# Performance work log

Measured on AMD Instinct MI355X. Metric: run time of the kernel, lower is better.

Reference implementation:

```python
import jax, jax.numpy as jnp
import numpy as np

G = 256       # number of graphs in batch
NPG = 400     # nodes per graph (hardcoded in module)
DEG = 32      # avg degree
FIN = 400     # input feature dim
H = 64        # hidden_channels
N = G * NPG
E = G * NPG * DEG


def _glorot(key, fan_in, fan_out):
    lim = float(np.sqrt(6.0 / (fan_in + fan_out)))
    return jax.random.uniform(key, (fan_in, fan_out), jnp.float32, -lim, lim)


def setup_inputs() -> dict:
    key = jax.random.key(0)
    ks = jax.random.split(key, 12)
    x = jax.random.normal(ks[0], (N, FIN), jnp.float32)
    # intra-graph random edges, then offset by graph id so edges never cross graphs
    src = jax.random.randint(ks[1], (G, NPG * DEG), 0, NPG)
    dst = jax.random.randint(ks[2], (G, NPG * DEG), 0, NPG)
    offs = (jnp.arange(G) * NPG)[:, None]
    edge_index = jnp.stack([(src + offs).reshape(-1), (dst + offs).reshape(-1)]).astype(jnp.int32)
    edge_weight = jax.random.uniform(ks[3], (E,), jnp.float32)
    return {
        "x": x,
        "edge_index": edge_index,
        "edge_weight": edge_weight,
        "W1": _glorot(ks[4], FIN, H), "b1": jnp.zeros((H,), jnp.float32),
        "W2": _glorot(ks[5], H, H),   "b2": jnp.zeros((H,), jnp.float32),
        "W3": _glorot(ks[6], H, H),   "b3": jnp.zeros((H,), jnp.float32),
        "Wc": _glorot(ks[7], NPG * H, H), "bc": jnp.zeros((H,), jnp.float32),
        "Wl": _glorot(ks[8], H, 2),   "bl": jnp.zeros((2,), jnp.float32),
    }


def _gcn_conv(x, W, b, row, col, norm, n):
    # PyG GCNConv: out[col] += norm * (x @ W)[row]; then + bias
    h = x @ W                                   # [n, out]
    msg = norm[:, None] * h[row]                # [E+n, out] gather + scale
    return jax.ops.segment_sum(msg, col, num_segments=n) + b


def reference(x, edge_index, edge_weight, W1, b1, W2, b2, W3, b3, Wc, bc, Wl, bl):
    n = x.shape[0]
    loop = jnp.arange(n, dtype=edge_index.dtype)
    row = jnp.concatenate([edge_index[0], loop])            # sources (with self-loops)
    col = jnp.concatenate([edge_index[1], loop])            # targets
    ew = jnp.concatenate([edge_weight, jnp.ones((n,), edge_weight.dtype)])
    # symmetric normalization: deg^{-1/2}[row] * w * deg^{-1/2}[col]
    deg = jax.ops.segment_sum(ew, col, num_segments=n)
    dinv = jnp.where(deg > 0, jax.lax.rsqrt(deg), 0.0)
    norm = dinv[row] * ew * dinv[col]

    h = jax.nn.relu(_gcn_conv(x, W1, b1, row, col, norm, n))
    h = jax.nn.relu(_gcn_conv(h, W2, b2, row, col, norm, n))
    h = _gcn_conv(h, W3, b3, row, col, norm, n)
    # per-graph flatten of 400 nodes -> lincomb (vectorized form of the Python loop)
    g = h.reshape(-1, NPG * H) @ Wc + bc        # [G, H]
    # dropout p=0.5 skipped (eval mode)
    return g @ Wl + bl                          # [G, 2]
```

## Files before the change

kernel.cpp:

```cpp
#include <hip/hip_runtime.h>
#include <hip/hip_bf16.h>
#include <stdint.h>

#define G 256
#define NPG 400
#define DEG 32
#define FIN 400
#define H 64
#define NN (G*NPG)
#define EE (G*NPG*DEG)
#define EPG (NPG*DEG)
#define CPG (EPG+NPG)
#define NTILE 25
#define ATS 420
#define HTS 72
#define MTF 26624

#define W1F_OFF 0
#define W1F_N   (13*4*64*8)
#define W2F_OFF (W1F_OFF + W1F_N)
#define W2F_N   (2*4*64*8)
#define W3F_OFF (W2F_OFF + W2F_N)
#define WCF_OFF (W3F_OFF + W2F_N)
#define WCF_N   (832*4*64*8)
#define WF_TOT  (WCF_OFF + WCF_N)

typedef __attribute__((ext_vector_type(8))) _Float16 h8;
typedef __attribute__((ext_vector_type(4))) float f32x4;

static __device__ __forceinline__ unsigned packh2(float a, float b) {
  unsigned short ua = __builtin_bit_cast(unsigned short, (_Float16)a);
  unsigned short ub = __builtin_bit_cast(unsigned short, (_Float16)b);
  return (unsigned)ua | ((unsigned)ub << 16);
}

static __device__ __forceinline__ h8 cvt8(float4 a, float4 b) {
  h8 r;
  r[0] = (_Float16)a.x; r[1] = (_Float16)a.y; r[2] = (_Float16)a.z; r[3] = (_Float16)a.w;
  r[4] = (_Float16)b.x; r[5] = (_Float16)b.y; r[6] = (_Float16)b.z; r[7] = (_Float16)b.w;
  return r;
}

__global__ __launch_bounds__(256) void kPack(
    const float* __restrict__ W1, const float* __restrict__ W2,
    const float* __restrict__ W3, const float* __restrict__ Wc,
    _Float16* __restrict__ wf)
{
  int idx = blockIdx.x*256 + threadIdx.x;
  if (idx >= WF_TOT) return;
  if (idx < W2F_OFF) {
    int i = idx;
    int j = i & 7, ln = (i >> 3) & 63, nt = (i >> 9) & 3, ks = i >> 11;
    int k = ks*32 + (ln >> 4)*8 + j, col = nt*16 + (ln & 15);
    wf[idx] = (k < FIN) ? (_Float16)W1[k*H + col] : (_Float16)0.f;
  } else if (idx < W3F_OFF) {
    int i = idx - W2F_OFF;
    int j = i & 7, ln = (i >> 3) & 63, nt = (i >> 9) & 3, ks = i >> 11;
    wf[idx] = (_Float16)W2[(ks*32 + (ln >> 4)*8 + j)*H + nt*16 + (ln & 15)];
  } else if (idx < WCF_OFF) {
    int i = idx - W3F_OFF;
    int j = i & 7, ln = (i >> 3) & 63, nt = (i >> 9) & 3, ks = i >> 11;
    wf[idx] = (_Float16)W3[(ks*32 + (ln >> 4)*8 + j)*H + nt*16 + (ln & 15)];
  } else {
    int i = idx - WCF_OFF;
    int j = i & 7, ln = (i >> 3) & 63, ntc = (i >> 9) & 3, kt = i >> 11;
    int kp = kt*32 + (ln >> 4)*8 + j;
    int nt_m = kp / 6656, rem = kp % 6656;
    int ks_m = rem >> 9, rem2 = rem & 511;
    int lane_m = rem2 >> 3, j_m = rem2 & 7;
    int node = ks_m*32 + (lane_m >> 4)*8 + j_m;
    int feat = nt_m*16 + (lane_m & 15);
    int col = ntc*16 + (ln & 15);
    wf[idx] = (node < NPG) ? (_Float16)Wc[((size_t)node*64 + feat)*64 + col]
                           : (_Float16)0.f;
  }
}

__global__ __launch_bounds__(1024) void kNorm(
    const int* __restrict__ ei, const float* __restrict__ ew,
    uint2* __restrict__ ent, uint32_t* __restrict__ boff)
{
  __shared__ float deg[NPG];
  __shared__ float dv[NPG];
  __shared__ uint32_t bcnt[32], bpos[32];
  const int g = blockIdx.x, tid = threadIdx.x;
  const int ebase = g*EPG, nbase = g*NPG;
  const int* rowp = ei;
  const int* colp = ei + EE;
  if (tid < NTILE) bcnt[tid] = 0u;
  for (int v = tid; v < NPG; v += 1024) deg[v] = 1.0f;
  __syncthreads();
  for (int e = tid; e < EPG; e += 1024) {
    int c = colp[ebase+e] - nbase;
    atomicAdd(&deg[c], ew[ebase+e]);
    atomicAdd(&bcnt[c >> 4], 1u);
  }
  __syncthreads();
  for (int v = tid; v < NPG; v += 1024) dv[v] = rsqrtf(deg[v]);
  if (tid == 0) {
    uint32_t s = 0;
    #pragma unroll
    for (int t = 0; t < NTILE; ++t) {
      uint32_t c = bcnt[t] + 16u;
      bcnt[t] = s; bpos[t] = s; s += c;
    }
  }
  __syncthreads();
  if (tid < NTILE) boff[g*32 + tid] = bcnt[tid];
  if (tid == NTILE) boff[g*32 + NTILE] = (uint32_t)CPG;
  uint2* eb = ent + (size_t)g*CPG;
  for (int e = tid; e < EPG; e += 1024) {
    int src = rowp[ebase+e] - nbase;
    int dst = colp[ebase+e] - nbase;
    float nm = dv[src] * ew[ebase+e] * dv[dst];
    uint32_t p = atomicAdd(&bpos[dst >> 4], 1u);
    eb[p] = make_uint2(((unsigned)dst << 16) | (unsigned)src, __float_as_uint(nm));
  }
  for (int v = tid; v < NPG; v += 1024) {
    uint32_t p = atomicAdd(&bpos[v >> 4], 1u);
    eb[p] = make_uint2(((unsigned)v << 16) | (unsigned)v, __float_as_uint(dv[v]*dv[v]));
  }
}

__global__ __launch_bounds__(256, 8) void kM1(
    const float* __restrict__ x, const _Float16* __restrict__ wf,
    _Float16* __restrict__ mt1)
{
  const int tid = threadIdx.x, lane = tid & 63, wave = tid >> 6;
  const int l15 = lane & 15, kgrp = lane >> 4;
  const int g = blockIdx.y, b = blockIdx.x;
  const int node_l = b*64 + wave*16 + l15;
  const int arow = (node_l < NPG) ? node_l : NPG-1;
  const float* xp = x + ((size_t)g*NPG + arow)*FIN;

  f32x4 acc[4] = {{0,0,0,0},{0,0,0,0},{0,0,0,0},{0,0,0,0}};
  for (int ks = 0; ks < 13; ++ks) {
    const int kb = ks*32 + kgrp*8;
    h8 af;
    if (kb + 8 <= FIN) {
      float4 a0 = *(const float4*)(xp + kb);
      float4 a1 = *(const float4*)(xp + kb + 4);
      af = cvt8(a0, a1);
    } else {
      h8 z;
      #pragma unroll
      for (int j = 0; j < 8; ++j) z[j] = (_Float16)0.f;
      af = z;
    }
    #pragma unroll
    for (int nt = 0; nt < 4; ++nt) {
      h8 bf = *(const h8*)&wf[W1F_OFF + (((size_t)ks*4 + nt)*64 + lane)*8];
      acc[nt] = __builtin_amdgcn_mfma_f32_16x16x32_f16(af, bf, acc[nt], 0, 0, 0);
    }
  }
  const int nd0 = b*64 + wave*16 + kgrp*4;
  if (nd0 < NPG) {
    const int ksw = nd0 >> 5, lh = (nd0 >> 3) & 3, jb = nd0 & 7;
    _Float16* mb = mt1 + (size_t)g*MTF;
    #pragma unroll
    for (int nt = 0; nt < 4; ++nt) {
      uint2 u;
      u.x = packh2(acc[nt][0], acc[nt][1]);
      u.y = packh2(acc[nt][2], acc[nt][3]);
      *(uint2*)&mb[(((size_t)nt*13 + ksw)*64 + lh*16 + l15)*8 + jb] = u;
    }
  }
}

template<int WMUL>
__global__ __launch_bounds__(256, 4) void kAgg(
    const _Float16* __restrict__ mtin, const _Float16* __restrict__ wfn,
    const float* __restrict__ bias,
    const uint2* __restrict__ ent, const uint32_t* __restrict__ boff,
    _Float16* __restrict__ out)
{
  extern __shared__ char smem[];
  float* sAT = (float*)smem;
  _Float16* sh = (_Float16*)(smem + 16*ATS*4);
  const int tid = threadIdx.x, lane = tid & 63;
  const int l15 = lane & 15, kgrp = lane >> 4;
  const int bid = blockIdx.x;
  const int g = bid & 255, t = bid >> 8;
  const int t0 = t*16;
  const int nt = tid >> 6;
  const uint2* eb = ent + (size_t)g*CPG;
  const uint32_t s0 = boff[g*32 + t], s1 = boff[g*32 + t + 1];

  h8 BF[13];
  const _Float16* mrow = mtin + (size_t)g*MTF + (size_t)nt*13*512 + lane*8;
  #pragma unroll
  for (int ks = 0; ks < 13; ++ks)
    BF[ks] = *(const h8*)(mrow + ks*512);
  const float bv = bias[nt*16 + l15];
  h8 WF2[2];
  if (WMUL) {
    WF2[0] = *(const h8*)&wfn[((size_t)(0*4 + nt)*64 + lane)*8];
    WF2[1] = *(const h8*)&wfn[((size_t)(1*4 + nt)*64 + lane)*8];
  }
  const uint32_t e0 = s0 + tid;
  uint2 E0 = make_uint2(0,0), E1 = make_uint2(0,0), E2 = make_uint2(0,0);
  if (e0       < s1) E0 = eb[e0];
  if (e0 + 256 < s1) E1 = eb[e0 + 256];
  if (e0 + 512 < s1) E2 = eb[e0 + 512];

  { float4* p = (float4*)sAT;
    for (int i = tid; i < 16*ATS/4; i += 256) p[i] = make_float4(0,0,0,0); }
  __syncthreads();

  if (e0       < s1) atomicAdd(&sAT[((int)(E0.x >> 16) - t0)*ATS + (int)(E0.x & 0xffffu)], __uint_as_float(E0.y));
  if (e0 + 256 < s1) atomicAdd(&sAT[((int)(E1.x >> 16) - t0)*ATS + (int)(E1.x & 0xffffu)], __uint_as_float(E1.y));
  if (e0 + 512 < s1) atomicAdd(&sAT[((int)(E2.x >> 16) - t0)*ATS + (int)(E2.x & 0xffffu)], __uint_as_float(E2.y));
  for (uint32_t e = e0 + 768; e < s1; e += 256) {
    uint2 E = eb[e];
    atomicAdd(&sAT[((int)(E.x >> 16) - t0)*ATS + (int)(E.x & 0xffffu)], __uint_as_float(E.y));
  }
  __syncthreads();

  f32x4 acc = {0,0,0,0};
  const float* ap = &sAT[l15*ATS];
  #pragma unroll
  for (int ks = 0; ks < 13; ++ks) {
    int kb = ks*32 + kgrp*8;
    float4 a0 = *(const float4*)(ap + kb);
    float4 a1 = *(const float4*)(ap + kb + 4);
    acc = __builtin_amdgcn_mfma_f32_16x16x32_f16(cvt8(a0, a1), BF[ks], acc, 0, 0, 0);
  }

  const int nd0 = t0 + kgrp*4;
  const int ksw = nd0 >> 5, lh = (nd0 >> 3) & 3, jb = nd0 & 7;
  _Float16* ob = out + (size_t)g*MTF;

  if (!WMUL) {
    uint2 u;
    u.x = packh2(acc[0] + bv, acc[1] + bv);
    u.y = packh2(acc[2] + bv, acc[3] + bv);
    *(uint2*)&ob[(((size_t)nt*13 + ksw)*64 + lh*16 + l15)*8 + jb] = u;
  } else {
    #pragma unroll
    for (int r = 0; r < 4; ++r)
      sh[(kgrp*4 + r)*HTS + nt*16 + l15] = (_Float16)fmaxf(acc[r] + bv, 0.f);
    __syncthreads();
    f32x4 acc2 = {0,0,0,0};
    const _Float16* hp = &sh[l15*HTS];
    acc2 = __builtin_amdgcn_mfma_f32_16x16x32_f16(*(const h8*)(hp + kgrp*8),      WF2[0], acc2, 0, 0, 0);
    acc2 = __builtin_amdgcn_mfma_f32_16x16x32_f16(*(const h8*)(hp + 32 + kgrp*8), WF2[1], acc2, 0, 0, 0);
    uint2 u;
    u.x = packh2(acc2[0], acc2[1]);
    u.y = packh2(acc2[2], acc2[3]);
    *(uint2*)&ob[(((size_t)nt*13 + ksw)*64 + lh*16 + l15)*8 + jb] = u;
  }
}

__global__ __launch_bounds__(256) void kRead(
    const _Float16* __restrict__ h3, const _Float16* __restrict__ wfc,
    float* __restrict__ gpart)
{
  const int tid = threadIdx.x, lane = tid & 63, nt = tid >> 6;
  const int l15 = lane & 15, kgrp = lane >> 4;
  const int rt = blockIdx.x & 15, kc = blockIdx.x >> 4;
  f32x4 acc = {0,0,0,0};
  const _Float16* hp = h3 + (size_t)(rt*16 + l15)*MTF;
  for (int ks = 0; ks < 26; ++ks) {
    int kt = kc*26 + ks;
    h8 af = *(const h8*)(hp + kt*32 + kgrp*8);
    h8 bf = *(const h8*)(wfc + (((size_t)kt*4 + nt)*64 + lane)*8);
    acc = __builtin_amdgcn_mfma_f32_16x16x32_f16(af, bf, acc, 0, 0, 0);
  }
  #pragma unroll
  for (int r = 0; r < 4; ++r)
    gpart[((size_t)(kc*16 + rt)*16 + kgrp*4 + r)*64 + nt*16 + l15] = acc[r];
}

__global__ __launch_bounds__(64) void k6_final(
    const float* __restrict__ gpart, const float* __restrict__ bc,
    const float* __restrict__ Wl, const float* __restrict__ bl,
    float* __restrict__ out)
{
  const int g = blockIdx.x, f = threadIdx.x;
  float s = bc[f];
  #pragma unroll 4
  for (int kc = 0; kc < 32; ++kc)
    s += gpart[((size_t)(kc*16 + (g >> 4))*16 + (g & 15))*64 + f];
  float p0 = s * Wl[f*2 + 0];
  float p1 = s * Wl[f*2 + 1];
  #pragma unroll
  for (int d = 1; d < 64; d <<= 1) {
    p0 += __shfl_xor(p0, d);
    p1 += __shfl_xor(p1, d);
  }
  if (f == 0) {
    out[g*2 + 0] = p0 + bl[0];
    out[g*2 + 1] = p1 + bl[1];
  }
}

extern "C" void kernel_launch(void* const* d_in, const int* in_sizes, int n_in,
                              void* d_out, int out_size, void* d_ws, size_t ws_size,
                              hipStream_t stream)
{
  const float* x  = (const float*)d_in[0];
  const int*   ei = (const int*)d_in[1];
  const float* ew = (const float*)d_in[2];
  const float* W1 = (const float*)d_in[3];
  const float* b1 = (const float*)d_in[4];
  const float* W2 = (const float*)d_in[5];
  const float* b2 = (const float*)d_in[6];
  const float* W3 = (const float*)d_in[7];
  const float* b3 = (const float*)d_in[8];
  const float* Wc = (const float*)d_in[9];
  const float* bc = (const float*)d_in[10];
  const float* Wl = (const float*)d_in[11];
  const float* bl = (const float*)d_in[12];
  float* out = (float*)d_out;
  (void)ws_size;

  char* ws = (char*)d_ws;
  size_t o = 0;
  uint2*     ent   = (uint2*)(ws + o);     o += (size_t)G*CPG*8;
  uint32_t*  boff  = (uint32_t*)(ws + o);  o += (size_t)G*32*4;
  _Float16*  mtA   = (_Float16*)(ws + o);  o += (size_t)G*MTF*2 + 256;
  _Float16*  mtB   = (_Float16*)(ws + o);  o += (size_t)G*MTF*2 + 256;
  _Float16*  wf    = (_Float16*)(ws + o);  o += (size_t)WF_TOT*2;
  float*     gpart = (float*)(ws + o);     o += (size_t)32*G*H*4;

  kPack<<<WF_TOT/256, 256, 0, stream>>>(W1, W2, W3, Wc, wf);
  kNorm<<<G, 1024, 0, stream>>>(ei, ew, ent, boff);
  kM1<<<dim3(7, G), 256, 0, stream>>>(x, wf, mtA);
  const int aggLds = 16*ATS*4 + 16*HTS*2;
  kAgg<1><<<NTILE*G, 256, aggLds, stream>>>(mtA, wf + W2F_OFF, b1, ent, boff, mtB);
  kAgg<1><<<NTILE*G, 256, aggLds, stream>>>(mtB, wf + W3F_OFF, b2, ent, boff, mtA);
  kAgg<0><<<NTILE*G, 256, aggLds, stream>>>(mtA, wf, b3, ent, boff, mtB);
  kRead<<<512, 256, 0, stream>>>(mtB, wf + WCF_OFF, gpart);
  k6_final<<<G, 64, 0, stream>>>(gpart, bc, Wl, bl, out);
}
```

Before: 265.6 us.

## Compress edge entries to 32 bits, coalesce x loads via LDS, split Wc packing

```diff
diff --git a/kernel.cpp b/kernel.cpp
--- a/kernel.cpp
+++ b/kernel.cpp
@@ -14,6 +14,7 @@
 #define NTILE 25
 #define ATS 420
 #define HTS 72
+#define XTS 36
 #define MTF 26624
 
 #define W1F_OFF 0
@@ -41,13 +42,12 @@
   return r;
 }
 
-__global__ __launch_bounds__(256) void kPack(
+__global__ __launch_bounds__(256) void kPackW(
     const float* __restrict__ W1, const float* __restrict__ W2,
-    const float* __restrict__ W3, const float* __restrict__ Wc,
-    _Float16* __restrict__ wf)
+    const float* __restrict__ W3, _Float16* __restrict__ wf)
 {
   int idx = blockIdx.x*256 + threadIdx.x;
-  if (idx >= WF_TOT) return;
+  if (idx >= WCF_OFF) return;
   if (idx < W2F_OFF) {
     int i = idx;
     int j = i & 7, ln = (i >> 3) & 63, nt = (i >> 9) & 3, ks = i >> 11;
@@ -57,28 +57,41 @@
     int i = idx - W2F_OFF;
     int j = i & 7, ln = (i >> 3) & 63, nt = (i >> 9) & 3, ks = i >> 11;
     wf[idx] = (_Float16)W2[(ks*32 + (ln >> 4)*8 + j)*H + nt*16 + (ln & 15)];
-  } else if (idx < WCF_OFF) {
+  } else {
     int i = idx - W3F_OFF;
     int j = i & 7, ln = (i >> 3) & 63, nt = (i >> 9) & 3, ks = i >> 11;
     wf[idx] = (_Float16)W3[(ks*32 + (ln >> 4)*8 + j)*H + nt*16 + (ln & 15)];
-  } else {
-    int i = idx - WCF_OFF;
-    int j = i & 7, ln = (i >> 3) & 63, ntc = (i >> 9) & 3, kt = i >> 11;
-    int kp = kt*32 + (ln >> 4)*8 + j;
-    int nt_m = kp / 6656, rem = kp % 6656;
+  }
+}
+
+__global__ __launch_bounds__(256) void kPackC(
+    const float* __restrict__ Wc, _Float16* __restrict__ wf)
+{
+  __shared__ _Float16 st[2048];
+  const int kt = blockIdx.x, tid = threadIdx.x;
+  #pragma unroll
+  for (int it = 0; it < 8; ++it) {
+    int r = it*4 + (tid >> 6);
+    int col = tid & 63;
+    int kp = kt*32 + r;
+    int nt_m = kp/6656, rem = kp%6656;
     int ks_m = rem >> 9, rem2 = rem & 511;
     int lane_m = rem2 >> 3, j_m = rem2 & 7;
     int node = ks_m*32 + (lane_m >> 4)*8 + j_m;
     int feat = nt_m*16 + (lane_m & 15);
-    int col = ntc*16 + (ln & 15);
-    wf[idx] = (node < NPG) ? (_Float16)Wc[((size_t)node*64 + feat)*64 + col]
-                           : (_Float16)0.f;
-  }
+    float v = (node < NPG) ? Wc[((size_t)node*64 + feat)*64 + col] : 0.f;
+    int dst = (col >> 4)*512 + (((r >> 3)*16 + (col & 15)))*8 + (r & 7);
+    st[dst] = (_Float16)v;
+  }
+  __syncthreads();
+  const uint4* s4 = (const uint4*)st;
+  uint4* d4 = (uint4*)(wf + WCF_OFF + (size_t)kt*2048);
+  d4[tid] = s4[tid];
 }
 
 __global__ __launch_bounds__(1024) void kNorm(
     const int* __restrict__ ei, const float* __restrict__ ew,
-    uint2* __restrict__ ent, uint32_t* __restrict__ boff)
+    uint32_t* __restrict__ ent, uint32_t* __restrict__ boff)
 {
   __shared__ float deg[NPG];
   __shared__ float dv[NPG];
@@ -108,17 +121,20 @@
   __syncthreads();
   if (tid < NTILE) boff[g*32 + tid] = bcnt[tid];
   if (tid == NTILE) boff[g*32 + NTILE] = (uint32_t)CPG;
-  uint2* eb = ent + (size_t)g*CPG;
+  uint32_t* eb = ent + (size_t)g*CPG;
   for (int e = tid; e < EPG; e += 1024) {
     int src = rowp[ebase+e] - nbase;
     int dst = colp[ebase+e] - nbase;
     float nm = dv[src] * ew[ebase+e] * dv[dst];
+    unsigned short nb = __builtin_bit_cast(unsigned short, (_Float16)nm);
     uint32_t p = atomicAdd(&bpos[dst >> 4], 1u);
-    eb[p] = make_uint2(((unsigned)dst << 16) | (unsigned)src, __float_as_uint(nm));
+    eb[p] = ((unsigned)(dst & 15) << 26) | ((unsigned)src << 16) | nb;
   }
   for (int v = tid; v < NPG; v += 1024) {
+    float nm = dv[v]*dv[v];
+    unsigned short nb = __builtin_bit_cast(unsigned short, (_Float16)nm);
     uint32_t p = atomicAdd(&bpos[v >> 4], 1u);
-    eb[p] = make_uint2(((unsigned)v << 16) | (unsigned)v, __float_as_uint(dv[v]*dv[v]));
+    eb[p] = ((unsigned)(v & 15) << 26) | ((unsigned)v << 16) | nb;
   }
 }
 
@@ -126,27 +142,26 @@
     const float* __restrict__ x, const _Float16* __restrict__ wf,
     _Float16* __restrict__ mt1)
 {
+  __shared__ float sx[64*XTS];
   const int tid = threadIdx.x, lane = tid & 63, wave = tid >> 6;
   const int l15 = lane & 15, kgrp = lane >> 4;
   const int g = blockIdx.y, b = blockIdx.x;
-  const int node_l = b*64 + wave*16 + l15;
-  const int arow = (node_l < NPG) ? node_l : NPG-1;
-  const float* xp = x + ((size_t)g*NPG + arow)*FIN;
+  const int rr = tid >> 2, ro = (tid & 3)*4;
+  const int srow = (b*64 + rr < NPG) ? (b*64 + rr) : (NPG - 1);
+  const float* xrow = x + ((size_t)g*NPG + srow)*FIN;
 
   f32x4 acc[4] = {{0,0,0,0},{0,0,0,0},{0,0,0,0},{0,0,0,0}};
   for (int ks = 0; ks < 13; ++ks) {
-    const int kb = ks*32 + kgrp*8;
-    h8 af;
-    if (kb + 8 <= FIN) {
-      float4 a0 = *(const float4*)(xp + kb);
-      float4 a1 = *(const float4*)(xp + kb + 4);
-      af = cvt8(a0, a1);
-    } else {
-      h8 z;
-      #pragma unroll
-      for (int j = 0; j < 8; ++j) z[j] = (_Float16)0.f;
-      af = z;
-    }
+    const int kb = ks*32;
+    const float4 z4 = make_float4(0.f, 0.f, 0.f, 0.f);
+    float4 v0 = (kb + ro + 4  <= FIN) ? *(const float4*)(xrow + kb + ro)      : z4;
+    float4 v1 = (kb + ro + 20 <= FIN) ? *(const float4*)(xrow + kb + ro + 16) : z4;
+    __syncthreads();
+    *(float4*)&sx[rr*XTS + ro]      = v0;
+    *(float4*)&sx[rr*XTS + ro + 16] = v1;
+    __syncthreads();
+    const float* ap = &sx[(wave*16 + l15)*XTS + kgrp*8];
+    h8 af = cvt8(*(const float4*)ap, *(const float4*)(ap + 4));
     #pragma unroll
     for (int nt = 0; nt < 4; ++nt) {
       h8 bf = *(const h8*)&wf[W1F_OFF + (((size_t)ks*4 + nt)*64 + lane)*8];
@@ -171,7 +186,7 @@
 __global__ __launch_bounds__(256, 4) void kAgg(
     const _Float16* __restrict__ mtin, const _Float16* __restrict__ wfn,
     const float* __restrict__ bias,
-    const uint2* __restrict__ ent, const uint32_t* __restrict__ boff,
+    const uint32_t* __restrict__ ent, const uint32_t* __restrict__ boff,
     _Float16* __restrict__ out)
 {
   extern __shared__ char smem[];
@@ -181,9 +196,8 @@
   const int l15 = lane & 15, kgrp = lane >> 4;
   const int bid = blockIdx.x;
   const int g = bid & 255, t = bid >> 8;
-  const int t0 = t*16;
   const int nt = tid >> 6;
-  const uint2* eb = ent + (size_t)g*CPG;
+  const uint32_t* eb = ent + (size_t)g*CPG;
   const uint32_t s0 = boff[g*32 + t], s1 = boff[g*32 + t + 1];
 
   h8 BF[13];
@@ -198,21 +212,26 @@
     WF2[1] = *(const h8*)&wfn[((size_t)(1*4 + nt)*64 + lane)*8];
   }
   const uint32_t e0 = s0 + tid;
-  uint2 E0 = make_uint2(0,0), E1 = make_uint2(0,0), E2 = make_uint2(0,0);
-  if (e0       < s1) E0 = eb[e0];
-  if (e0 + 256 < s1) E1 = eb[e0 + 256];
-  if (e0 + 512 < s1) E2 = eb[e0 + 512];
+  uint32_t E0 = 0, E1 = 0, E2 = 0;
+  bool p0 = e0 < s1, p1 = e0 + 256 < s1, p2 = e0 + 512 < s1;
+  if (p0) E0 = eb[e0];
+  if (p1) E1 = eb[e0 + 256];
+  if (p2) E2 = eb[e0 + 512];
 
   { float4* p = (float4*)sAT;
     for (int i = tid; i < 16*ATS/4; i += 256) p[i] = make_float4(0,0,0,0); }
   __syncthreads();
 
-  if (e0       < s1) atomicAdd(&sAT[((int)(E0.x >> 16) - t0)*ATS + (int)(E0.x & 0xffffu)], __uint_as_float(E0.y));
-  if (e0 + 256 < s1) atomicAdd(&sAT[((int)(E1.x >> 16) - t0)*ATS + (int)(E1.x & 0xffffu)], __uint_as_float(E1.y));
-  if (e0 + 512 < s1) atomicAdd(&sAT[((int)(E2.x >> 16) - t0)*ATS + (int)(E2.x & 0xffffu)], __uint_as_float(E2.y));
+  if (p0) atomicAdd(&sAT[(int)(E0 >> 26)*ATS + (int)((E0 >> 16) & 0x3FFu)],
+                    (float)__builtin_bit_cast(_Float16, (unsigned short)(E0 & 0xFFFFu)));
+  if (p1) atomicAdd(&sAT[(int)(E1 >> 26)*ATS + (int)((E1 >> 16) & 0x3FFu)],
+                    (float)__builtin_bit_cast(_Float16, (unsigned short)(E1 & 0xFFFFu)));
+  if (p2) atomicAdd(&sAT[(int)(E2 >> 26)*ATS + (int)((E2 >> 16) & 0x3FFu)],
+                    (float)__builtin_bit_cast(_Float16, (unsigned short)(E2 & 0xFFFFu)));
   for (uint32_t e = e0 + 768; e < s1; e += 256) {
-    uint2 E = eb[e];
-    atomicAdd(&sAT[((int)(E.x >> 16) - t0)*ATS + (int)(E.x & 0xffffu)], __uint_as_float(E.y));
+    uint32_t E = eb[e];
+    atomicAdd(&sAT[(int)(E >> 26)*ATS + (int)((E >> 16) & 0x3FFu)],
+              (float)__builtin_bit_cast(_Float16, (unsigned short)(E & 0xFFFFu)));
   }
   __syncthreads();
 
@@ -226,7 +245,7 @@
     acc = __builtin_amdgcn_mfma_f32_16x16x32_f16(cvt8(a0, a1), BF[ks], acc, 0, 0, 0);
   }
 
-  const int nd0 = t0 + kgrp*4;
+  const int nd0 = t*16 + kgrp*4;
   const int ksw = nd0 >> 5, lh = (nd0 >> 3) & 3, jb = nd0 & 7;
   _Float16* ob = out + (size_t)g*MTF;
 
@@ -316,14 +335,15 @@
 
   char* ws = (char*)d_ws;
   size_t o = 0;
-  uint2*     ent   = (uint2*)(ws + o);     o += (size_t)G*CPG*8;
+  uint32_t*  ent   = (uint32_t*)(ws + o);  o += (size_t)G*CPG*4;
   uint32_t*  boff  = (uint32_t*)(ws + o);  o += (size_t)G*32*4;
   _Float16*  mtA   = (_Float16*)(ws + o);  o += (size_t)G*MTF*2 + 256;
   _Float16*  mtB   = (_Float16*)(ws + o);  o += (size_t)G*MTF*2 + 256;
   _Float16*  wf    = (_Float16*)(ws + o);  o += (size_t)WF_TOT*2;
   float*     gpart = (float*)(ws + o);     o += (size_t)32*G*H*4;
 
-  kPack<<<WF_TOT/256, 256, 0, stream>>>(W1, W2, W3, Wc, wf);
+  kPackW<<<(WCF_OFF+255)/256, 256, 0, stream>>>(W1, W2, W3, wf);
+  kPackC<<<832, 256, 0, stream>>>(Wc, wf);
   kNorm<<<G, 1024, 0, stream>>>(ei, ew, ent, boff);
   kM1<<<dim3(7, G), 256, 0, stream>>>(x, wf, mtA);
   const int aggLds = 16*ATS*4 + 16*HTS*2;
```

Measured after the change: 284.2 us. +7.0%, slower.
